# Performance work log

Hardware: AMD Instinct MI355X
Metric: run time of the kernel (lower is better)

## Reference

```python
import jax, jax.numpy as jnp
import numpy as np

ALPHA = 0.2  # LeakyReLU negative slope
NEG_BIG = -9e15


def setup_inputs() -> dict:
    key = jax.random.key(0)
    k1, k2, k3, k4 = jax.random.split(key, 4)
    B, N, Fin, Fout = 16, 1024, 256, 256
    h = jax.random.normal(k1, (B, N, Fin), dtype=jnp.float32)
    adj = jax.random.randint(k2, (B, N, N), 0, 2, dtype=jnp.int32)
    # xavier_uniform with gain=1.414
    def xavier(k, shape, gain=1.414):
        fan_in, fan_out = shape[0], shape[1]
        bound = gain * np.sqrt(6.0 / (fan_in + fan_out))
        return jax.random.uniform(k, shape, jnp.float32, -bound, bound)
    W = xavier(k3, (Fin, Fout))
    a = xavier(k4, (2 * Fout, 1))
    return {"h": h, "adj": adj, "W": W, "a": a}


def reference(h, adj, W, a):
    # h: [B,N,Fin], adj: [B,N,N], W: [Fin,Fout], a: [2*Fout,1]
    Fout = W.shape[1]
    Wh = jnp.einsum('bnf,fo->bno', h, W)                      # [B,N,Fout]
    a1, a2 = a[:Fout, 0], a[Fout:, 0]                          # [Fout], [Fout]
    # e_ij = leakyrelu(Wh_i . a1 + Wh_j . a2) -- outer sum, no O(N^2*F) tensor
    f1 = Wh @ a1                                               # [B,N]
    f2 = Wh @ a2                                               # [B,N]
    e = jax.nn.leaky_relu(f1[:, :, None] + f2[:, None, :], negative_slope=ALPHA)
    attention = jnp.where(adj > 0, e, jnp.float32(NEG_BIG))    # [B,N,N]
    attention = jax.nn.softmax(attention, axis=2)
    h_prime = jnp.einsum('bij,bjo->bio', attention, Wh)        # [B,N,Fout]
    return jax.nn.elu(h_prime)
```

## Files before the change

kernel.cpp:

```cpp
#include <hip/hip_runtime.h>
#include <hip/hip_bf16.h>

#define Bsz 16
#define Nn  1024
#define Ff  256
#define ALPHA 0.2f
#define NEG_BIG -9.0e15f

typedef __attribute__((ext_vector_type(8))) short short8;
typedef __attribute__((ext_vector_type(4))) float f32x4;
typedef __attribute__((ext_vector_type(4))) unsigned short ushort4_t;

__device__ __forceinline__ unsigned short f2bf(float x) {
    union { __hip_bfloat16 b; unsigned short u; } cv;
    cv.b = __float2bfloat16(x);
    return cv.u;
}

__global__ __launch_bounds__(256) void gat_prep(
    const float* __restrict__ W, const float* __restrict__ a,
    float* __restrict__ w1, float* __restrict__ w2,
    unsigned short* __restrict__ WK)
{
    const int t = threadIdx.x, w = t >> 6, ln = t & 63;
    if (blockIdx.x < 64) {
        __shared__ float a1s[Ff], a2s[Ff];
        a1s[t] = a[t];
        a2s[t] = a[Ff + t];
        __syncthreads();
        const int f = blockIdx.x * 4 + w;
        float s1 = 0.f, s2 = 0.f;
        #pragma unroll
        for (int c = 0; c < 4; c++) {
            const int o = ln + 64 * c;
            const float wv = W[(size_t)f * Ff + o];
            s1 += wv * a1s[o];
            s2 += wv * a2s[o];
        }
        #pragma unroll
        for (int off = 1; off < 64; off <<= 1) {
            s1 += __shfl_xor(s1, off, 64);
            s2 += __shfl_xor(s2, off, 64);
        }
        if (ln == 0) { w1[f] = s1; w2[f] = s2; }
        return;
    }
    __shared__ __align__(16) float tile[32][258];
    const int ft = blockIdx.x - 64;
    const float* src = W + (size_t)ft * 32 * Ff;
    #pragma unroll
    for (int rr = 0; rr < 8; rr++) {
        const int row = rr * 4 + w;
        const int col = ln * 4;
        const float4 v = *(const float4*)&src[row * Ff + col];
        float2* tr = (float2*)&tile[row][col];
        tr[0] = make_float2(v.x, v.y);
        tr[1] = make_float2(v.z, v.w);
    }
    __syncthreads();
    unsigned* d32 = (unsigned*)(WK + (size_t)ft * 8192);
    #pragma unroll
    for (int k = 0; k < 16; k++) {
        const int fidx = k * 256 + t;
        const int o = fidx >> 4, q = fidx & 15;
        const unsigned lo = f2bf(tile[2 * q][o]);
        const unsigned hi = f2bf(tile[2 * q + 1][o]);
        d32[fidx] = lo | (hi << 16);
    }
}

__global__ __launch_bounds__(256) void pack_f(
    const float* __restrict__ h, const unsigned short* __restrict__ WK,
    const float* __restrict__ w1, const float* __restrict__ w2,
    unsigned short* __restrict__ WhK,
    float* __restrict__ f1, float* __restrict__ f2)
{
    __shared__ __align__(16) float tile[32][258];
    const int id = blockIdx.x, t = threadIdx.x, w = t >> 6, ln = t & 63;
    const int grow0 = id * 32;
    const float* src = h + (size_t)grow0 * Ff;
    #pragma unroll
    for (int rr = 0; rr < 8; rr++) {
        const int row = rr * 4 + w;
        const int col = ln * 4;
        const float4 v = *(const float4*)&src[row * Ff + col];
        float2* tr = (float2*)&tile[row][col];
        tr[0] = make_float2(v.x, v.y);
        tr[1] = make_float2(v.z, v.w);
    }
    __syncthreads();

    {
        float w1r[4], w2r[4];
        #pragma unroll
        for (int c = 0; c < 4; c++) {
            w1r[c] = w1[ln + 64 * c];
            w2r[c] = w2[ln + 64 * c];
        }
        #pragma unroll
        for (int rr = 0; rr < 8; rr++) {
            const int row = rr * 4 + w;
            float s1 = 0.f, s2 = 0.f;
            #pragma unroll
            for (int c = 0; c < 4; c++) {
                const float hv = tile[row][ln + 64 * c];
                s1 += hv * w1r[c];
                s2 += hv * w2r[c];
            }
            #pragma unroll
            for (int off = 1; off < 64; off <<= 1) {
                s1 += __shfl_xor(s1, off, 64);
                s2 += __shfl_xor(s2, off, 64);
            }
            if (ln == 0) { f1[grow0 + row] = s1; f2[grow0 + row] = s2; }
        }
    }

    const int m = ln & 15, quad = ln >> 4;
    f32x4 acc0[4], acc1[4];
    #pragma unroll
    for (int nt = 0; nt < 4; nt++) {
        f32x4 z = {0.f, 0.f, 0.f, 0.f};
        acc0[nt] = z; acc1[nt] = z;
    }
    #pragma unroll
    for (int kt = 0; kt < 8; kt++) {
        short8 a0, a1;
        {
            const float* p0 = &tile[m][kt * 32 + quad * 8];
            const float* p1 = &tile[16 + m][kt * 32 + quad * 8];
            #pragma unroll
            for (int e = 0; e < 8; e++) {
                a0[e] = (short)f2bf(p0[e]);
                a1[e] = (short)f2bf(p1[e]);
            }
        }
        #pragma unroll
        for (int nt = 0; nt < 4; nt++) {
            const short8 bfr = *(const short8*)&WK[(size_t)kt * 8192 + (w * 64 + nt * 16 + m) * 32 + quad * 8];
            acc0[nt] = __builtin_amdgcn_mfma_f32_16x16x32_bf16(a0, bfr, acc0[nt], 0, 0, 0);
            acc1[nt] = __builtin_amdgcn_mfma_f32_16x16x32_bf16(a1, bfr, acc1[nt], 0, 0, 0);
        }
    }
    unsigned short* dst = WhK + (size_t)id * 8192;
    #pragma unroll
    for (int nt = 0; nt < 4; nt++) {
        const int o = w * 64 + nt * 16 + m;
        ushort4_t v0 = { f2bf(acc0[nt][0]), f2bf(acc0[nt][1]),
                         f2bf(acc0[nt][2]), f2bf(acc0[nt][3]) };
        ushort4_t v1 = { f2bf(acc1[nt][0]), f2bf(acc1[nt][1]),
                         f2bf(acc1[nt][2]), f2bf(acc1[nt][3]) };
        *(ushort4_t*)&dst[o * 32 + quad * 4]      = v0;
        *(ushort4_t*)&dst[o * 32 + 16 + quad * 4] = v1;
    }
}

#define TI 32
#define PST 1040
__global__ __launch_bounds__(1024, 8) void gat_attn(
    const int* __restrict__ adj,
    const float* __restrict__ f1, const float* __restrict__ f2,
    const unsigned short* __restrict__ WhK,
    float* __restrict__ out)
{
    __shared__ __align__(16) unsigned short pbf[TI * PST];
    const int t = threadIdx.x, w = t >> 6, ln = t & 63;
    const int m = ln & 15, quad = ln >> 4;
    const int bid = blockIdx.x;
    const int b  = 2 * (bid & 7) + ((bid >> 3) & 1);
    const int i0 = (bid >> 4) * TI;

    const int r0 = 2 * w, r1 = r0 + 1;
    const int grb = b * Nn + i0 + r0;
    const int* aptr = adj + (size_t)grb * Nn;
    int4 av0[4], av1[4];
    #pragma unroll
    for (int c = 0; c < 4; c++) {
        av0[c] = *(const int4*)&aptr[c * 256 + 4 * ln];
        av1[c] = *(const int4*)&aptr[Nn + c * 256 + 4 * ln];
    }
    float4 f2r[4];
    #pragma unroll
    for (int c = 0; c < 4; c++)
        f2r[c] = *(const float4*)&f2[b * Nn + 256 * c + 4 * ln];

    const float fi0 = f1[grb], fi1 = f1[grb + 1];
    float e0[16], e1[16];
    float mx0 = -INFINITY, mx1 = -INFINITY;
    #pragma unroll
    for (int c = 0; c < 4; c++) {
        const float4 fv = f2r[c];
        float x, y;
        x = fi0 + fv.x; x = fmaxf(x, ALPHA * x); x = av0[c].x > 0 ? x : NEG_BIG; e0[4*c+0] = x;
        y = fi0 + fv.y; y = fmaxf(y, ALPHA * y); y = av0[c].y > 0 ? y : NEG_BIG; e0[4*c+1] = y;
        mx0 = fmaxf(fmaxf(x, y), mx0);
        x = fi0 + fv.z; x = fmaxf(x, ALPHA * x); x = av0[c].z > 0 ? x : NEG_BIG; e0[4*c+2] = x;
        y = fi0 + fv.w; y = fmaxf(y, ALPHA * y); y = av0[c].w > 0 ? y : NEG_BIG; e0[4*c+3] = y;
        mx0 = fmaxf(fmaxf(x, y), mx0);
        x = fi1 + fv.x; x = fmaxf(x, ALPHA * x); x = av1[c].x > 0 ? x : NEG_BIG; e1[4*c+0] = x;
        y = fi1 + fv.y; y = fmaxf(y, ALPHA * y); y = av1[c].y > 0 ? y : NEG_BIG; e1[4*c+1] = y;
        mx1 = fmaxf(fmaxf(x, y), mx1);
        x = fi1 + fv.z; x = fmaxf(x, ALPHA * x); x = av1[c].z > 0 ? x : NEG_BIG; e1[4*c+2] = x;
        y = fi1 + fv.w; y = fmaxf(y, ALPHA * y); y = av1[c].w > 0 ? y : NEG_BIG; e1[4*c+3] = y;
        mx1 = fmaxf(fmaxf(x, y), mx1);
    }
    #pragma unroll
    for (int off = 1; off < 64; off <<= 1) {
        mx0 = fmaxf(mx0, __shfl_xor(mx0, off, 64));
        mx1 = fmaxf(mx1, __shfl_xor(mx1, off, 64));
    }
    float s0 = 0.f, s1 = 0.f;
    #pragma unroll
    for (int c = 0; c < 16; c++) {
        e0[c] = __expf(e0[c] - mx0); s0 += e0[c];
        e1[c] = __expf(e1[c] - mx1); s1 += e1[c];
    }
    #pragma unroll
    for (int off = 1; off < 64; off <<= 1) {
        s0 += __shfl_xor(s0, off, 64);
        s1 += __shfl_xor(s1, off, 64);
    }
    const float ri0 = 1.f / s0, ri1 = 1.f / s1;
    const int sw0 = (r0 & 7) << 3, sw1 = (r1 & 7) << 3;
    #pragma unroll
    for (int c = 0; c < 4; c++) {
        const int j = 256 * c + 4 * ln;
        ushort4_t v0 = { f2bf(e0[4*c] * ri0), f2bf(e0[4*c+1] * ri0),
                         f2bf(e0[4*c+2] * ri0), f2bf(e0[4*c+3] * ri0) };
        ushort4_t v1 = { f2bf(e1[4*c] * ri1), f2bf(e1[4*c+1] * ri1),
                         f2bf(e1[4*c+2] * ri1), f2bf(e1[4*c+3] * ri1) };
        *(ushort4_t*)&pbf[r0 * PST + (j ^ sw0)] = v0;
        *(ushort4_t*)&pbf[r1 * PST + (j ^ sw1)] = v1;
    }

    const int n0 = w * 16;
    const unsigned short* hKb = WhK + (size_t)b * 32 * 8192;
    const int arow0 = m * PST, arow1 = (16 + m) * PST;
    const int asw = (m & 7) << 3;
    #define AF0(kt) (*(const short8*)&pbf[arow0 + ((((kt) * 32) + quad * 8) ^ asw)])
    #define AF1(kt) (*(const short8*)&pbf[arow1 + ((((kt) * 32) + quad * 8) ^ asw)])
    #define BF(kt)  (*(const short8*)&hKb[(size_t)(kt) * 8192 + (n0 + m) * 32 + quad * 8])

    short8 bq0 = BF(0), bq1 = BF(1), bq2 = BF(2), bq3 = BF(3);
    __syncthreads();

    f32x4 acc0 = {0.f, 0.f, 0.f, 0.f}, acc1 = acc0;
    short8 a0c = AF0(0), a1c = AF1(0);
    __builtin_amdgcn_s_setprio(1);
    #pragma unroll
    for (int kt = 0; kt < 32; kt++) {
        short8 bnew = bq0, a0n = a0c, a1n = a1c;
        if (kt + 4 < 32) bnew = BF(kt + 4);
        if (kt + 1 < 32) { a0n = AF0(kt + 1); a1n = AF1(kt + 1); }
        acc0 = __builtin_amdgcn_mfma_f32_16x16x32_bf16(a0c, bq0, acc0, 0, 0, 0);
        acc1 = __builtin_amdgcn_mfma_f32_16x16x32_bf16(a1c, bq0, acc1, 0, 0, 0);
        a0c = a0n; a1c = a1n;
        bq0 = bq1; bq1 = bq2; bq2 = bq3; bq3 = bnew;
    }
    __builtin_amdgcn_s_setprio(0);

    const size_t ob = (size_t)(b * Nn) + i0;
    #pragma unroll
    for (int reg = 0; reg < 4; reg++) {
        float v;
        v = acc0[reg]; v = v > 0.f ? v : (__expf(v) - 1.f);
        out[(ob + quad * 4 + reg) * Ff + n0 + m] = v;
        v = acc1[reg]; v = v > 0.f ? v : (__expf(v) - 1.f);
        out[(ob + 16 + quad * 4 + reg) * Ff + n0 + m] = v;
    }
}

extern "C" void kernel_launch(void* const* d_in, const int* in_sizes, int n_in,
                              void* d_out, int out_size, void* d_ws, size_t ws_size,
                              hipStream_t stream)
{
    const void* h   = d_in[0];
    const void* adj = d_in[1];
    const void* W   = d_in[2];
    const void* a   = d_in[3];
    for (int i = 0; i < n_in; i++) {
        if      (in_sizes[i] == Bsz * Nn * Ff) h   = d_in[i];
        else if (in_sizes[i] == Bsz * Nn * Nn) adj = d_in[i];
        else if (in_sizes[i] == Ff * Ff)       W   = d_in[i];
        else if (in_sizes[i] == 2 * Ff)        a   = d_in[i];
    }
    float* out = (float*)d_out;

    char*  wsb = (char*)d_ws;
    float* w1  = (float*)wsb;
    float* w2  = w1 + Ff;
    float* f1  = (float*)(wsb + 4096);
    float* f2  = f1 + Bsz * Nn;
    unsigned short* WhK = (unsigned short*)(wsb + 4096 + 2 * 65536);
    unsigned short* WK  = WhK + (size_t)Bsz * 32 * 8192;

    gat_prep<<<72, 256, 0, stream>>>((const float*)W, (const float*)a, w1, w2, WK);
    pack_f<<<512, 256, 0, stream>>>((const float*)h, WK, w1, w2, WhK, f1, f2);
    gat_attn<<<Bsz * (Nn / TI), 1024, 0, stream>>>((const int*)adj, f1, f2, WhK, out);
}
```

Measured before the change: 139.8 us.

## Fuse W/a preprocessing into the pack kernel, removing one launch

Merges the gat_prep kernel into the Wh packing kernel. Each of the 512 blocks now reads W directly, converts it to bf16 in shared memory per k-tile, and recomputes w1=W·a1 and w2=W·a2 locally. This removes one kernel launch and the global round-trip for WK, w1 and w2. In exchange it adds redundant W reads and reductions in every block, two syncthreads per k-iteration, and extra shared memory (16KB plus 2KB), which may lower occupancy.

```diff
diff --git a/kernel.cpp b/kernel.cpp
--- a/kernel.cpp
+++ b/kernel.cpp
@@ -17,37 +17,19 @@
     return cv.u;
 }
 
-__global__ __launch_bounds__(256) void gat_prep(
-    const float* __restrict__ W, const float* __restrict__ a,
-    float* __restrict__ w1, float* __restrict__ w2,
-    unsigned short* __restrict__ WK)
+__global__ __launch_bounds__(256) void k_pack(
+    const float* __restrict__ h, const float* __restrict__ W,
+    const float* __restrict__ a,
+    unsigned short* __restrict__ WhK,
+    float* __restrict__ f1, float* __restrict__ f2)
 {
-    const int t = threadIdx.x, w = t >> 6, ln = t & 63;
-    if (blockIdx.x < 64) {
-        __shared__ float a1s[Ff], a2s[Ff];
-        a1s[t] = a[t];
-        a2s[t] = a[Ff + t];
-        __syncthreads();
-        const int f = blockIdx.x * 4 + w;
-        float s1 = 0.f, s2 = 0.f;
-        #pragma unroll
-        for (int c = 0; c < 4; c++) {
-            const int o = ln + 64 * c;
-            const float wv = W[(size_t)f * Ff + o];
-            s1 += wv * a1s[o];
-            s2 += wv * a2s[o];
-        }
-        #pragma unroll
-        for (int off = 1; off < 64; off <<= 1) {
-            s1 += __shfl_xor(s1, off, 64);
-            s2 += __shfl_xor(s2, off, 64);
-        }
-        if (ln == 0) { w1[f] = s1; w2[f] = s2; }
-        return;
-    }
     __shared__ __align__(16) float tile[32][258];
-    const int ft = blockIdx.x - 64;
-    const float* src = W + (size_t)ft * 32 * Ff;
+    __shared__ __align__(16) unsigned wk32[4096];
+    __shared__ float w1s[Ff], w2s[Ff];
+    const int bid = blockIdx.x, t = threadIdx.x, w = t >> 6, ln = t & 63;
+
+    const int grow0 = bid * 32;
+    const float* src = h + (size_t)grow0 * Ff;
     #pragma unroll
     for (int rr = 0; rr < 8; rr++) {
         const int row = rr * 4 + w;
@@ -57,45 +39,95 @@
         tr[0] = make_float2(v.x, v.y);
         tr[1] = make_float2(v.z, v.w);
     }
+
+    const int q  = t >> 4;
+    const int og = t & 15;
+    float4 a1r[4], a2r[4];
+    #pragma unroll
+    for (int i = 0; i < 4; i++) {
+        a1r[i] = *(const float4*)&a[og * 16 + 4 * i];
+        a2r[i] = *(const float4*)&a[Ff + og * 16 + 4 * i];
+    }
     __syncthreads();
-    unsigned* d32 = (unsigned*)(WK + (size_t)ft * 8192);
-    #pragma unroll
-    for (int k = 0; k < 16; k++) {
-        const int fidx = k * 256 + t;
-        const int o = fidx >> 4, q = fidx & 15;
-        const unsigned lo = f2bf(tile[2 * q][o]);
-        const unsigned hi = f2bf(tile[2 * q + 1][o]);
-        d32[fidx] = lo | (hi << 16);
-    }
-}
-
-__global__ __launch_bounds__(256) void pack_f(
-    const float* __restrict__ h, const unsigned short* __restrict__ WK,
-    const float* __restrict__ w1, const float* __restrict__ w2,
-    unsigned short* __restrict__ WhK,
-    float* __restrict__ f1, float* __restrict__ f2)
-{
-    __shared__ __align__(16) float tile[32][258];
-    const int id = blockIdx.x, t = threadIdx.x, w = t >> 6, ln = t & 63;
-    const int grow0 = id * 32;
-    const float* src = h + (size_t)grow0 * Ff;
-    #pragma unroll
-    for (int rr = 0; rr < 8; rr++) {
-        const int row = rr * 4 + w;
-        const int col = ln * 4;
-        const float4 v = *(const float4*)&src[row * Ff + col];
-        float2* tr = (float2*)&tile[row][col];
-        tr[0] = make_float2(v.x, v.y);
-        tr[1] = make_float2(v.z, v.w);
-    }
-    __syncthreads();
+
+    const int m = ln & 15, quad = ln >> 4;
+    f32x4 acc0[4], acc1[4];
+    #pragma unroll
+    for (int nt = 0; nt < 4; nt++) {
+        f32x4 z = {0.f, 0.f, 0.f, 0.f};
+        acc0[nt] = z; acc1[nt] = z;
+    }
+    const unsigned short* wkus = (const unsigned short*)wk32;
+
+    for (int kt = 0; kt < 8; kt++) {
+        const int rowA = kt * 32 + 2 * q;
+        const float* wa = W + (size_t)rowA * Ff + og * 16;
+        const float* wb = wa + Ff;
+        float4 A[4], B[4];
+        #pragma unroll
+        for (int i = 0; i < 4; i++) {
+            A[i] = *(const float4*)&wa[4 * i];
+            B[i] = *(const float4*)&wb[4 * i];
+        }
+        float s1A = 0.f, s2A = 0.f, s1B = 0.f, s2B = 0.f;
+        #pragma unroll
+        for (int i = 0; i < 4; i++) {
+            s1A += A[i].x * a1r[i].x + A[i].y * a1r[i].y + A[i].z * a1r[i].z + A[i].w * a1r[i].w;
+            s2A += A[i].x * a2r[i].x + A[i].y * a2r[i].y + A[i].z * a2r[i].z + A[i].w * a2r[i].w;
+            s1B += B[i].x * a1r[i].x + B[i].y * a1r[i].y + B[i].z * a1r[i].z + B[i].w * a1r[i].w;
+            s2B += B[i].x * a2r[i].x + B[i].y * a2r[i].y + B[i].z * a2r[i].z + B[i].w * a2r[i].w;
+        }
+        #pragma unroll
+        for (int off = 1; off < 16; off <<= 1) {
+            s1A += __shfl_xor(s1A, off, 64);
+            s2A += __shfl_xor(s2A, off, 64);
+            s1B += __shfl_xor(s1B, off, 64);
+            s2B += __shfl_xor(s2B, off, 64);
+        }
+        if (og == 0) {
+            w1s[rowA] = s1A; w1s[rowA + 1] = s1B;
+            w2s[rowA] = s2A; w2s[rowA + 1] = s2B;
+        }
+        #pragma unroll
+        for (int i = 0; i < 4; i++) {
+            const int ob = og * 16 + 4 * i;
+            wk32[(ob + 0) * 16 + q] = (unsigned)f2bf(A[i].x) | ((unsigned)f2bf(B[i].x) << 16);
+            wk32[(ob + 1) * 16 + q] = (unsigned)f2bf(A[i].y) | ((unsigned)f2bf(B[i].y) << 16);
+            wk32[(ob + 2) * 16 + q] = (unsigned)f2bf(A[i].z) | ((unsigned)f2bf(B[i].z) << 16);
+            wk32[(ob + 3) * 16 + q] = (unsigned)f2bf(A[i].w) | ((unsigned)f2bf(B[i].w) << 16);
+        }
+        __syncthreads();
+
+        short8 a0, a1v;
+        {
+            const float* p0 = &tile[m][kt * 32 + quad * 8];
+            const float* p1 = &tile[16 + m][kt * 32 + quad * 8];
+            #pragma unroll
+            for (int e = 0; e < 8; e++) {
+                a0[e]  = (short)f2bf(p0[e]);
+                a1v[e] = (short)f2bf(p1[e]);
+            }
+        }
+        #pragma unroll
+        for (int nt = 0; nt < 4; nt++) {
+            const short8 bfr = *(const short8*)&wkus[(w * 64 + nt * 16 + m) * 32 + quad * 8];
+            acc0[nt] = __builtin_amdgcn_mfma_f32_16x16x32_bf16(a0,  bfr, acc0[nt], 0, 0, 0);
+            acc1[nt] = __builtin_amdgcn_mfma_f32_16x16x32_bf16(a1v, bfr, acc1[nt], 0, 0, 0);
+        }
+        __syncthreads();
+    }
 
     {
         float w1r[4], w2r[4];
         #pragma unroll
         for (int c = 0; c < 4; c++) {
-            w1r[c] = w1[ln + 64 * c];
-            w2r[c] = w2[ln + 64 * c];
+            w1r[c] = w1s[ln + 64 * c];
+            w2r[c] = w2s[ln + 64 * c];
+        }
+        #pragma unroll
+        for (int rr = 0; rr < 2; rr++) {
+            const int row = 2 * w + rr;
+            (void)row;
         }
         #pragma unroll
         for (int rr = 0; rr < 8; rr++) {
@@ -116,33 +148,7 @@
         }
     }
 
-    const int m = ln & 15, quad = ln >> 4;
-    f32x4 acc0[4], acc1[4];
-    #pragma unroll
-    for (int nt = 0; nt < 4; nt++) {
-        f32x4 z = {0.f, 0.f, 0.f, 0.f};
-        acc0[nt] = z; acc1[nt] = z;
-    }
-    #pragma unroll
-    for (int kt = 0; kt < 8; kt++) {
-        short8 a0, a1;
-        {
-            const float* p0 = &tile[m][kt * 32 + quad * 8];
-            const float* p1 = &tile[16 + m][kt * 32 + quad * 8];
-            #pragma unroll
-            for (int e = 0; e < 8; e++) {
-                a0[e] = (short)f2bf(p0[e]);
-                a1[e] = (short)f2bf(p1[e]);
-            }
-        }
-        #pragma unroll
-        for (int nt = 0; nt < 4; nt++) {
-            const short8 bfr = *(const short8*)&WK[(size_t)kt * 8192 + (w * 64 + nt * 16 + m) * 32 + quad * 8];
-            acc0[nt] = __builtin_amdgcn_mfma_f32_16x16x32_bf16(a0, bfr, acc0[nt], 0, 0, 0);
-            acc1[nt] = __builtin_amdgcn_mfma_f32_16x16x32_bf16(a1, bfr, acc1[nt], 0, 0, 0);
-        }
-    }
-    unsigned short* dst = WhK + (size_t)id * 8192;
+    unsigned short* dst = WhK + (size_t)bid * 8192;
     #pragma unroll
     for (int nt = 0; nt < 4; nt++) {
         const int o = w * 64 + nt * 16 + m;
@@ -284,17 +290,13 @@
         else if (in_sizes[i] == Ff * Ff)       W   = d_in[i];
         else if (in_sizes[i] == 2 * Ff)        a   = d_in[i];
     }
-    float* out = (float*)d_out;
-
-    char*  wsb = (char*)d_ws;
-    float* w1  = (float*)wsb;
-    float* w2  = w1 + Ff;
-    float* f1  = (float*)(wsb + 4096);
-    float* f2  = f1 + Bsz * Nn;
-    unsigned short* WhK = (unsigned short*)(wsb + 4096 + 2 * 65536);
-    unsigned short* WK  = WhK + (size_t)Bsz * 32 * 8192;
-
-    gat_prep<<<72, 256, 0, stream>>>((const float*)W, (const float*)a, w1, w2, WK);
-    pack_f<<<512, 256, 0, stream>>>((const float*)h, WK, w1, w2, WhK, f1, f2);
-    gat_attn<<<Bsz * (Nn / TI), 1024, 0, stream>>>((const int*)adj, f1, f2, WhK, out);
+    char* wsb = (char*)d_ws;
+    float* f1 = (float*)wsb;
+    float* f2 = (float*)(wsb + 65536);
+    unsigned short* WhK = (unsigned short*)(wsb + 131072);
+
+    k_pack<<<512, 256, 0, stream>>>((const float*)h, (const float*)W,
+                                    (const float*)a, WhK, f1, f2);
+    gat_attn<<<Bsz * (Nn / TI), 1024, 0, stream>>>((const int*)adj, f1, f2,
+                                                   WhK, (float*)d_out);
 }
```

Measured after the change: 158.4 us. 1.13x slower.
